# Performance work log

Measured on AMD Instinct MI355X. Metric: run time of the kernel, lower is better.

## Reference

```python
import jax, jax.numpy as jnp
import numpy as np

TS = 7           # tile_size
STRIDE = 3       # tile_size - overlap
RATIO = 4
C = 4            # margs.channel
S_LR = 256       # ms side
S_HR = 1024      # margs.test_sidelen
N_ATOMS = 10
TSR = TS * RATIO
STR_R = STRIDE * RATIO
NP_SIDE = (S_LR - TS) // STRIDE + 1   # 84 (pad_size == 0 for this config)
NPATCH = NP_SIDE ** 2                 # 7056


def unfold(x, k, stride):
    # x: [1,C,H,W] -> [1, C*k*k, N]  (channel-major patch layout, same as torch F.unfold)
    p = jax.lax.conv_general_dilated_patches(x, (k, k), (stride, stride), 'VALID')
    return p.reshape(1, p.shape[1], -1)


def fold(p, c, h, w, k, stride):
    # F.fold is the adjoint (overlap-add transpose) of unfold
    _, vjp = jax.vjp(lambda x: unfold(x, k, stride), jnp.zeros((1, c, h, w), p.dtype))
    return vjp(p)[0]


def _gauss(k, sigma):
    ax = np.arange(k) - (k - 1) / 2.0
    g = np.exp(-ax ** 2 / (2.0 * sigma ** 2))
    g = g / g.sum()
    return jnp.asarray(np.outer(g, g), dtype=jnp.float32)


def wald(x, ratio):
    # wald_protocol low-pass: depthwise gaussian blur (MTF approximation)
    k = 4 * ratio + 1
    ker = jnp.broadcast_to(_gauss(k, float(ratio)), (x.shape[1], 1, k, k))
    return jax.lax.conv_general_dilated(x, ker, (1, 1), 'SAME', feature_group_count=x.shape[1])


def setup_inputs() -> dict:
    key = jax.random.key(0)
    ks = jax.random.split(key, 4)
    # histogram-matched PAN high-pass (C channels, matched per band)
    pan_hp = jax.random.normal(ks[0], (1, C, S_HR, S_HR), jnp.float32)
    lr_pan_hp = wald(pan_hp, RATIO)[:, :, 2:-1:4, 2:-1:4]          # [1,C,256,256]
    lr_dict = unfold(lr_pan_hp, TS, STRIDE)[0].T                    # [NPATCH, C*TS^2]
    hr_dict = unfold(pan_hp, TSR, STR_R)[0].T                       # [NPATCH, C*TSR^2]
    ms_hp = 0.1 * jax.random.normal(ks[1], (1, C, S_LR, S_LR), jnp.float32)
    lms = jax.random.normal(ks[2], (1, C, S_HR, S_HR), jnp.float32)
    hrms_hp = 0.1 * jax.random.normal(ks[3], (1, C, S_HR, S_HR), jnp.float32)
    divisor = fold(jnp.ones((1, C * TSR * TSR, NPATCH), jnp.float32), C, S_HR, S_HR, TSR, STR_R)
    divisor = jnp.where(divisor == 0, 1.0, divisor)
    return {"hrms_hp": hrms_hp, "ms_hp": ms_hp, "lms": lms,
            "lr_dict": lr_dict, "hr_dict": hr_dict, "divisor": divisor}


def reference(hrms_hp, ms_hp, lms, lr_dict, hr_dict, divisor):
    N = lr_dict.shape[0]
    hw = TS * TS
    hwr = TSR * TSR
    # residual MS patches: ms_hp - degraded current estimate
    lr_hrms = wald(hrms_hp, RATIO)[:, :, 2:-1:4, 2:-1:4]
    res_ms = unfold(ms_hp - lr_hrms, TS, STRIDE)[0]                 # [C*hw, N]
    res_ms = res_ms.reshape(C, hw, N).transpose(2, 0, 1).reshape(N * C, hw)  # '(n c) hw'
    res = res_ms.reshape(N, C * hw)                                 # 'n (c hw)'
    idx_cols = [jnp.arange(N)]                                      # index[:,0] = arange
    alpha = None
    for i in range(N_ATOMS):
        if i > 0:
            # greedy atom selection: max |<residual, atom>|
            idx_cols.append(jnp.argmax(jnp.abs(res @ lr_dict.T), axis=-1))
        idx = jnp.stack(idx_cols, axis=1)                           # [N, i+1]
        A = lr_dict[idx]                                            # [N, i+1, C*hw]
        A = A.reshape(N, i + 1, C, hw).transpose(0, 2, 3, 1).reshape(N * C, hw, i + 1)
        # batched least squares (min-norm, matches torch.linalg.lstsq)
        alpha = jnp.einsum('bij,bj->bi', jnp.linalg.pinv(A), res_ms)  # [N*C, i+1]
        res = (res_ms - jnp.einsum('bi,bpi->bp', alpha, A)).reshape(N, C * hw)
    idx = jnp.stack(idx_cols, axis=1)                               # [N, N_ATOMS]
    Hd = hr_dict[idx].reshape(N, N_ATOMS, C, hwr).transpose(0, 2, 1, 3).reshape(N * C, N_ATOMS, hwr)
    hr_p = jnp.einsum('bi,bip->bp', alpha, Hd)                      # [N*C, hwr]
    hr_p = hr_p.reshape(N, C, hwr).transpose(1, 2, 0).reshape(1, C * hwr, N)
    hrms_out = fold(hr_p, C, S_HR, S_HR, TSR, STR_R) / (divisor + 1e-8) + hrms_hp
    return hrms_out + lms
```

## Files before the change

### kernel.cpp

```cpp
#include <hip/hip_runtime.h>
#include <math.h>

#define NP    7056
#define NP2   7168
#define NPS   84
#define CCH   4
#define HW    49
#define HWR   784
#define KF    196
#define KSEG  196
#define KC    608
#define NH    19
#define NA    10
#define SLR   256
#define GK    17

typedef _Float16 half8 __attribute__((ext_vector_type(8)));
typedef float f32x4 __attribute__((ext_vector_type(4)));

__global__ void hpass_kernel(const float* __restrict__ hr, float* __restrict__ htmp) {
    __shared__ float g[GK];
    int tid = threadIdx.x;
    if (tid < GK) {
        double s = 0.0, mine = 0.0;
        for (int k = 0; k < GK; k++) {
            double ax = (double)k - 8.0;
            double e = exp(-ax * ax / 32.0);
            s += e;
            if (k == tid) mine = e;
        }
        g[tid] = (float)(mine / s);
    }
    __syncthreads();
    int gid = blockIdx.x * 256 + tid;
    int xs = gid & 255;
    int y  = (gid >> 8) & 1023;
    int c  = gid >> 18;
    const float* row = hr + (size_t)(c * 1024 + y) * 1024;
    int xb = xs * 4 - 6;
    float acc = 0.f;
#pragma unroll
    for (int k = 0; k < GK; k++) {
        int xc = xb + k;
        float v = (xc >= 0 && xc < 1024) ? row[xc] : 0.f;
        acc = fmaf(g[k], v, acc);
    }
    htmp[gid] = acc;
}

__global__ void vpass_kernel(const float* __restrict__ htmp, const float* __restrict__ ms,
                             float* __restrict__ diff) {
    __shared__ float g[GK];
    int tid = threadIdx.x;
    if (tid < GK) {
        double s = 0.0, mine = 0.0;
        for (int k = 0; k < GK; k++) {
            double ax = (double)k - 8.0;
            double e = exp(-ax * ax / 32.0);
            s += e;
            if (k == tid) mine = e;
        }
        g[tid] = (float)(mine / s);
    }
    __syncthreads();
    int gid = blockIdx.x * 256 + tid;
    int xs = gid & 255;
    int ys = (gid >> 8) & 255;
    int c  = gid >> 16;
    int yb = ys * 4 - 6;
    float acc = 0.f;
#pragma unroll
    for (int k = 0; k < GK; k++) {
        int yc = yb + k;
        float v = (yc >= 0 && yc < 1024) ? htmp[(size_t)(c * 1024 + yc) * 256 + xs] : 0.f;
        acc = fmaf(g[k], v, acc);
    }
    diff[gid] = ms[gid] - acc;
}

__global__ void build_y_kernel(const float* __restrict__ diff, float* __restrict__ yb) {
    int gid = blockIdx.x * 256 + threadIdx.x;
    if (gid >= NP * CCH * HW) return;
    int p = gid % HW;
    int b = gid / HW;
    int c = b & 3;
    int n = b >> 2;
    int py = n / NPS, px = n % NPS;
    int dy = p / 7, dx = p % 7;
    yb[gid] = diff[(size_t)(c * SLR + py * 3 + dy) * SLR + px * 3 + dx];
}

__global__ void splitcat_kernel(const float* __restrict__ src, _Float16* __restrict__ Dcat) {
    int gid = blockIdx.x * 256 + threadIdx.x;
    int r = gid / 76, v8 = gid - r * 76;
    const float* srow = src + (size_t)r * KF;
    bool valid = (r < NP);
    half8 o;
#pragma unroll
    for (int e = 0; e < 8; e++) {
        int k = v8 * 8 + e;
        int seg = (k >= 392) ? 2 : (k >= 196 ? 1 : 0);
        int ks = k - seg * 196;
        float x = (valid && k < 588) ? srow[ks] : 0.f;
        _Float16 hi = (_Float16)x;
        o[e] = (seg == 1) ? (_Float16)(x - (float)hi) : hi;
    }
    *(half8*)&Dcat[(size_t)r * KC + v8 * 8] = o;
}

__global__ void hd16_kernel(const float* __restrict__ hr_dict, _Float16* __restrict__ hd) {
    int gid = blockIdx.x * 256 + threadIdx.x;
    if (gid >= (NP * CCH * HWR) / 8) return;
    const float4 a = *(const float4*)&hr_dict[(size_t)gid * 8];
    const float4 b = *(const float4*)&hr_dict[(size_t)gid * 8 + 4];
    half8 o;
    o[0] = (_Float16)a.x; o[1] = (_Float16)a.y; o[2] = (_Float16)a.z; o[3] = (_Float16)a.w;
    o[4] = (_Float16)b.x; o[5] = (_Float16)b.y; o[6] = (_Float16)b.z; o[7] = (_Float16)b.w;
    *(half8*)&hd[(size_t)gid * 8] = o;
}

__device__ __forceinline__ unsigned long long shfl_xor_u64(unsigned long long v, int m) {
    unsigned int lo = (unsigned int)v;
    unsigned int hi = (unsigned int)(v >> 32);
    lo = __shfl_xor(lo, m, 64);
    hi = __shfl_xor(hi, m, 64);
    return ((unsigned long long)hi << 32) | (unsigned long long)lo;
}

__device__ __forceinline__ void gload16(const void* g, void* l) {
    __builtin_amdgcn_global_load_lds((const __attribute__((address_space(1))) void*)(void*)g,
                                     (__attribute__((address_space(3))) void*)l, 16, 0, 0);
}

__global__ __launch_bounds__(512, 4) void mfma_argmax_kernel(
    const _Float16* __restrict__ Rcat, const _Float16* __restrict__ Dcat,
    unsigned long long* __restrict__ keys, int seg) {
    __shared__ __align__(16) _Float16 lds[3 * 12288];
    const int tid = threadIdx.x;
    const int lane = tid & 63;
    const int wave = tid >> 6;
    const int wm = wave >> 1;
    const int wn = wave & 1;

    int b0 = (int)blockIdx.x;
    int xcd = b0 & 7, w = b0 >> 3;
    int by = w % 28;
    int bx = xcd * 7 + w / 28;
    const int row0 = by * 256, col0 = bx * 128;

    const int lr = lane & 15, lk = lane >> 4;
    const int xk = (lk ^ ((lr >> 1) & 3)) * 8;
    const int aBase = (wm * 64 + lr) * 32 + xk;
    const int bBase = 8192 + (wn * 64 + lr) * 32 + xk;

    const int srow = wave * 16 + (lane >> 2);
    const int sc = ((lane & 3) ^ ((lane >> 3) & 3)) * 8;
    const _Float16* pA = Rcat + (size_t)(row0 + srow) * KC + sc;
    const _Float16* pB = Dcat + (size_t)(col0 + srow) * KC + sc;
    const int dA1 = wave * 512, dA2 = 4096 + wave * 512, dB = 8192 + wave * 512;

    auto STAGE = [&](int h) {
        int q = (h % 3) * 12288;
        int off = h * 32;
        gload16(pA + off, &lds[q + dA1]);
        gload16(pA + (size_t)128 * KC + off, &lds[q + dA2]);
        gload16(pB + off, &lds[q + dB]);
    };

    f32x4 acc[4][4];
#pragma unroll
    for (int u = 0; u < 4; u++)
#pragma unroll
        for (int v = 0; v < 4; v++) {
            f32x4 zz = {0.f, 0.f, 0.f, 0.f};
            acc[u][v] = zz;
        }

    STAGE(0);
    STAGE(1);

    for (int h = 0; h < NH; ++h) {
        const int q = (h % 3) * 12288;
        int hn = h + 2; if (hn > NH - 1) hn = NH - 1;

        asm volatile("s_waitcnt vmcnt(3)" ::: "memory");
        __builtin_amdgcn_s_barrier();

        STAGE(hn);

        half8 aF[4], bF[4];
#pragma unroll
        for (int u = 0; u < 4; ++u)
            aF[u] = *(const half8*)&lds[q + aBase + u * 512];
#pragma unroll
        for (int v = 0; v < 4; ++v)
            bF[v] = *(const half8*)&lds[q + bBase + v * 512];

        __builtin_amdgcn_s_setprio(1);
#pragma unroll
        for (int u = 0; u < 4; ++u)
#pragma unroll
            for (int v = 0; v < 4; ++v)
                acc[u][v] = __builtin_amdgcn_mfma_f32_16x16x32_f16(aF[u], bF[v], acc[u][v], 0, 0, 0);
        __builtin_amdgcn_s_setprio(0);

        asm volatile("s_waitcnt lgkmcnt(0)" ::: "memory");
    }
    asm volatile("s_waitcnt vmcnt(0)" ::: "memory");

    unsigned long long* kseg = keys + (size_t)seg * NP;
#pragma unroll
    for (int u = 0; u < 4; u++)
#pragma unroll
        for (int j = 0; j < 4; j++) {
            unsigned long long key = 0ull;
#pragma unroll
            for (int v = 0; v < 4; v++) {
                int gc = col0 + wn * 64 + v * 16 + lr;
                if (gc < NP) {
                    unsigned int bits = __float_as_uint(fabsf(acc[u][v][j]));
                    unsigned long long k2 = ((unsigned long long)bits << 32) |
                                            (unsigned long long)(0xFFFFFFFFu - (unsigned int)gc);
                    key = (k2 > key) ? k2 : key;
                }
            }
#pragma unroll
            for (int m = 1; m < 16; m <<= 1) {
                unsigned long long o = shfl_xor_u64(key, m);
                key = (o > key) ? o : key;
            }
            if (lr == 0) {
                int gr = row0 + wm * 64 + u * 16 + lk * 4 + j;
                if (gr < NP) atomicMax(kseg + gr, key);
            }
        }
}

template <int M>
__global__ __launch_bounds__(256) void solve_kernel(
    const float* __restrict__ yb, const float* __restrict__ dict,
    const unsigned long long* __restrict__ keys9,
    int* __restrict__ idxb, float* __restrict__ alphab,
    _Float16* __restrict__ Rcat) {
    int n = (blockIdx.x * 256 + threadIdx.x) >> 6;
    int lane = threadIdx.x & 63;
    int g = lane >> 4, t = lane & 15;

    int newidx = 0;
    if (M >= 2) newidx = (int)(0xFFFFFFFFu -
        (unsigned int)(keys9[(size_t)(M - 2) * NP + n] & 0xFFFFFFFFull));
    if (lane == 0) {
        if (M == 1) idxb[n * NA] = n;
        else        idxb[n * NA + (M - 1)] = newidx;
    }

    int id[M];
#pragma unroll
    for (int k = 0; k < M; k++)
        id[k] = (k == 0) ? n : ((M >= 2 && k == M - 1) ? newidx : idxb[n * NA + k]);

    const int b = n * CCH + g;
    const int base_c = g * HW;

    constexpr int TRI = M * (M + 1) / 2;
    float G[TRI];
    float rhs[M];
#pragma unroll
    for (int q = 0; q < TRI; q++) G[q] = 0.f;
#pragma unroll
    for (int k = 0; k < M; k++) rhs[k] = 0.f;

#pragma unroll
    for (int rep = 0; rep < 4; rep++) {
        int p = t + rep * 16;
        if (p < HW) {
            float a[M];
#pragma unroll
            for (int k = 0; k < M; k++)
                a[k] = dict[(size_t)id[k] * KF + base_c + p];
            float yp = yb[(size_t)b * HW + p];
#pragma unroll
            for (int k = 0; k < M; k++) {
                rhs[k] = fmaf(a[k], yp, rhs[k]);
#pragma unroll
                for (int l = 0; l <= k; l++)
                    G[k * (k + 1) / 2 + l] = fmaf(a[k], a[l], G[k * (k + 1) / 2 + l]);
            }
        }
    }

#pragma unroll
    for (int m = 1; m < 16; m <<= 1) {
#pragma unroll
        for (int q = 0; q < TRI; q++) G[q] += __shfl_xor(G[q], m, 64);
#pragma unroll
        for (int k = 0; k < M; k++) rhs[k] += __shfl_xor(rhs[k], m, 64);
    }

#pragma unroll
    for (int k = 0; k < M; k++) {
        float s = G[k * (k + 1) / 2 + k];
#pragma unroll
        for (int j = 0; j < k; j++) {
            float l = G[k * (k + 1) / 2 + j];
            s = fmaf(-l, l, s);
        }
        float inv = 1.0f / sqrtf(fmaxf(s, 1e-30f));
        G[k * (k + 1) / 2 + k] = inv;
#pragma unroll
        for (int r = k + 1; r < M; r++) {
            float tt = G[r * (r + 1) / 2 + k];
#pragma unroll
            for (int j = 0; j < k; j++)
                tt = fmaf(-G[r * (r + 1) / 2 + j], G[k * (k + 1) / 2 + j], tt);
            G[r * (r + 1) / 2 + k] = tt * inv;
        }
    }
#pragma unroll
    for (int k = 0; k < M; k++) {
        float tt = rhs[k];
#pragma unroll
        for (int j = 0; j < k; j++) tt = fmaf(-G[k * (k + 1) / 2 + j], rhs[j], tt);
        rhs[k] = tt * G[k * (k + 1) / 2 + k];
    }
#pragma unroll
    for (int k = M - 1; k >= 0; k--) {
        float tt = rhs[k];
#pragma unroll
        for (int j = k + 1; j < M; j++) tt = fmaf(-G[j * (j + 1) / 2 + k], rhs[j], tt);
        rhs[k] = tt * G[k * (k + 1) / 2 + k];
    }

    if (t == 0) {
#pragma unroll
        for (int k = 0; k < M; k++) alphab[(size_t)b * NA + k] = rhs[k];
    }

    if (M < NA) {
        _Float16* r0 = Rcat + (size_t)n * KC + base_c;
#pragma unroll
        for (int rep = 0; rep < 4; rep++) {
            int p = t + rep * 16;
            if (p < HW) {
                float s = yb[(size_t)b * HW + p];
#pragma unroll
                for (int k = 0; k < M; k++)
                    s = fmaf(-rhs[k], dict[(size_t)id[k] * KF + base_c + p], s);
                _Float16 hi = (_Float16)s;
                r0[p] = hi;
                r0[KSEG + p] = hi;
                r0[2 * KSEG + p] = (_Float16)(s - (float)hi);
            }
        }
    }
}

__global__ __launch_bounds__(256) void recon_kernel(
    const float* __restrict__ alphab, const int* __restrict__ idxb,
    const _Float16* __restrict__ hd, _Float16* __restrict__ hr_p) {
    int n = blockIdx.x;
    int tid = threadIdx.x;
    __shared__ float al[CCH * NA];
    __shared__ int idn[NA];
    if (tid < CCH * NA) al[tid] = alphab[(size_t)n * CCH * NA + tid];
    if (tid < NA) idn[tid] = idxb[n * NA + tid];
    __syncthreads();
    for (int v = tid; v < (CCH * HWR) / 8; v += 256) {
        int c = v / (HWR / 8);
        float s[8] = {0.f, 0.f, 0.f, 0.f, 0.f, 0.f, 0.f, 0.f};
#pragma unroll
        for (int k = 0; k < NA; k++) {
            half8 d = *(const half8*)&hd[(size_t)idn[k] * (CCH * HWR) + v * 8];
            float ak = al[c * NA + k];
#pragma unroll
            for (int e = 0; e < 8; e++) s[e] = fmaf(ak, (float)d[e], s[e]);
        }
        half8 o;
#pragma unroll
        for (int e = 0; e < 8; e++) o[e] = (_Float16)s[e];
        *(half8*)&hr_p[(size_t)n * (CCH * HWR) + v * 8] = o;
    }
}

__global__ __launch_bounds__(256) void fold2_kernel(
    const _Float16* __restrict__ hr_p, const float* __restrict__ divisor,
    const float* __restrict__ hrms, const float* __restrict__ lms,
    float* __restrict__ out) {
    int gid = blockIdx.x * 256 + threadIdx.x;
    int x  = gid & 1023;
    int yy = (gid >> 10) & 1023;
    int c  = gid >> 20;

    int t0 = yy - 27;
    int py0 = (t0 > 0) ? (t0 + 11) / 12 : 0;
    int py1 = min(83, yy / 12);
    int s0 = x - 27;
    int px0 = (s0 > 0) ? (s0 + 11) / 12 : 0;
    int px1 = min(83, x / 12);

    float acc = 0.f;
    for (int py = py0; py <= py1; py++) {
        int qy = yy - py * 12;
        for (int px = px0; px <= px1; px++) {
            int qx = x - px * 12;
            int n = py * NPS + px;
            acc += (float)hr_p[(size_t)n * (CCH * HWR) + c * HWR + qy * 28 + qx];
        }
    }
    out[gid] = acc / (divisor[gid] + 1e-8f) + hrms[gid] + lms[gid];
}

__global__ __launch_bounds__(256) void fold_final_kernel(
    const float* __restrict__ alphab, const int* __restrict__ idxb,
    const float* __restrict__ hr_dict, const float* __restrict__ divisor,
    const float* __restrict__ hrms, const float* __restrict__ lms,
    float* __restrict__ out) {
    int gid = blockIdx.x * 256 + threadIdx.x;
    int x  = gid & 1023;
    int yy = (gid >> 10) & 1023;
    int c  = gid >> 20;
    int t0 = yy - 27;
    int py0 = (t0 > 0) ? (t0 + 11) / 12 : 0;
    int py1 = min(83, yy / 12);
    int s0 = x - 27;
    int px0 = (s0 > 0) ? (s0 + 11) / 12 : 0;
    int px1 = min(83, x / 12);
    float acc = 0.f;
    for (int py = py0; py <= py1; py++) {
        int qy = yy - py * 12;
        for (int px = px0; px <= px1; px++) {
            int qx = x - px * 12;
            int n = py * NPS + px;
            const float* al = alphab + (size_t)(n * CCH + c) * NA;
            const int* idn = idxb + n * NA;
            int q = qy * 28 + qx;
            float s = 0.f;
#pragma unroll
            for (int k = 0; k < NA; k++)
                s = fmaf(al[k], hr_dict[(size_t)idn[k] * (CCH * HWR) + c * HWR + q], s);
            acc += s;
        }
    }
    out[gid] = acc / (divisor[gid] + 1e-8f) + hrms[gid] + lms[gid];
}

extern "C" void kernel_launch(void* const* d_in, const int* in_sizes, int n_in,
                              void* d_out, int out_size, void* d_ws, size_t ws_size,
                              hipStream_t stream) {
    const float* hrms    = (const float*)d_in[0];
    const float* ms      = (const float*)d_in[1];
    const float* lms     = (const float*)d_in[2];
    const float* lr_dict = (const float*)d_in[3];
    const float* hr_dict = (const float*)d_in[4];
    const float* divisor = (const float*)d_in[5];
    float* out = (float*)d_out;

    char* ws = (char*)d_ws;
    size_t off = 0;
    auto alloc = [&](size_t bytes) -> void* {
        void* p = ws + off;
        off += (bytes + 255) & ~(size_t)255;
        return p;
    };
    float* htmp   = (float*)alloc((size_t)4 * 1024 * 256 * 4);
    float* diff   = (float*)alloc((size_t)4 * 256 * 256 * 4);
    float* yb     = (float*)alloc((size_t)NP * CCH * HW * 4);
    float* alphab = (float*)alloc((size_t)NP * CCH * NA * 4);
    int*   idxb   = (int*)alloc((size_t)NP * NA * 4);
    unsigned long long* keys9 = (unsigned long long*)alloc((size_t)NP * 9 * 8);
    _Float16* Dcat = (_Float16*)alloc((size_t)NP2 * KC * 2);
    _Float16* Rcat = (_Float16*)alloc((size_t)NP2 * KC * 2);
    _Float16* hd16 = (_Float16*)alloc((size_t)NP * CCH * HWR * 2);
    _Float16* hr_p = (_Float16*)alloc((size_t)NP * CCH * HWR * 2);
    bool two_stage = (off <= ws_size);

    hpass_kernel<<<4096, 256, 0, stream>>>(hrms, htmp);
    vpass_kernel<<<1024, 256, 0, stream>>>(htmp, ms, diff);
    build_y_kernel<<<(NP * CCH * HW + 255) / 256, 256, 0, stream>>>(diff, yb);
    splitcat_kernel<<<(NP2 * 76) / 256, 256, 0, stream>>>(lr_dict, Dcat);
    hipMemsetAsync(keys9, 0, (size_t)NP * 9 * 8, stream);
    if (two_stage)
        hd16_kernel<<<((NP * CCH * HWR) / 8 + 255) / 256, 256, 0, stream>>>(hr_dict, hd16);

    int sblocks = NP / 4;
    for (int i = 0; i < NA; i++) {
        if (i > 0)
            mfma_argmax_kernel<<<1568, 512, 0, stream>>>(Rcat, Dcat, keys9, i - 1);
        switch (i + 1) {
            case 1:  solve_kernel<1><<<sblocks, 256, 0, stream>>>(yb, lr_dict, keys9, idxb, alphab, Rcat); break;
            case 2:  solve_kernel<2><<<sblocks, 256, 0, stream>>>(yb, lr_dict, keys9, idxb, alphab, Rcat); break;
            case 3:  solve_kernel<3><<<sblocks, 256, 0, stream>>>(yb, lr_dict, keys9, idxb, alphab, Rcat); break;
            case 4:  solve_kernel<4><<<sblocks, 256, 0, stream>>>(yb, lr_dict, keys9, idxb, alphab, Rcat); break;
            case 5:  solve_kernel<5><<<sblocks, 256, 0, stream>>>(yb, lr_dict, keys9, idxb, alphab, Rcat); break;
            case 6:  solve_kernel<6><<<sblocks, 256, 0, stream>>>(yb, lr_dict, keys9, idxb, alphab, Rcat); break;
            case 7:  solve_kernel<7><<<sblocks, 256, 0, stream>>>(yb, lr_dict, keys9, idxb, alphab, Rcat); break;
            case 8:  solve_kernel<8><<<sblocks, 256, 0, stream>>>(yb, lr_dict, keys9, idxb, alphab, Rcat); break;
            case 9:  solve_kernel<9><<<sblocks, 256, 0, stream>>>(yb, lr_dict, keys9, idxb, alphab, Rcat); break;
            case 10: solve_kernel<10><<<sblocks, 256, 0, stream>>>(yb, lr_dict, keys9, idxb, alphab, Rcat); break;
        }
    }

    if (two_stage) {
        recon_kernel<<<NP, 256, 0, stream>>>(alphab, idxb, hd16, hr_p);
        fold2_kernel<<<(4 * 1024 * 1024) / 256, 256, 0, stream>>>(hr_p, divisor, hrms, lms, out);
    } else {
        fold_final_kernel<<<(4 * 1024 * 1024) / 256, 256, 0, stream>>>(
            alphab, idxb, hr_dict, divisor, hrms, lms, out);
    }
}
```

Baseline: 1.089 ms.

## Load A fragments directly from global into registers, stage only B in LDS

The argmax GEMM kernel stops staging the residual (A) tile through LDS. Each wave now loads its A fragments straight from global memory into registers one k-step ahead, while only the dictionary (B) tile goes through a triple-buffered LDS ring via global_load_lds. LDS use per block drops from 3x12288 to 3x4096 halves, which cuts LDS traffic and may allow more resident blocks. The cost is uncoalesced global reads for A, with each row read by both wn waves, and the wait counts and sched barriers have to keep the prefetch ordering correct.

```diff
diff --git a/kernel.cpp b/kernel.cpp
--- a/kernel.cpp
+++ b/kernel.cpp
@@ -135,7 +135,7 @@
 __global__ __launch_bounds__(512, 4) void mfma_argmax_kernel(
     const _Float16* __restrict__ Rcat, const _Float16* __restrict__ Dcat,
     unsigned long long* __restrict__ keys, int seg) {
-    __shared__ __align__(16) _Float16 lds[3 * 12288];
+    __shared__ __align__(16) _Float16 lds[3 * 4096];
     const int tid = threadIdx.x;
     const int lane = tid & 63;
     const int wave = tid >> 6;
@@ -150,21 +150,23 @@
 
     const int lr = lane & 15, lk = lane >> 4;
     const int xk = (lk ^ ((lr >> 1) & 3)) * 8;
-    const int aBase = (wm * 64 + lr) * 32 + xk;
-    const int bBase = 8192 + (wn * 64 + lr) * 32 + xk;
-
-    const int srow = wave * 16 + (lane >> 2);
-    const int sc = ((lane & 3) ^ ((lane >> 3) & 3)) * 8;
-    const _Float16* pA = Rcat + (size_t)(row0 + srow) * KC + sc;
-    const _Float16* pB = Dcat + (size_t)(col0 + srow) * KC + sc;
-    const int dA1 = wave * 512, dA2 = 4096 + wave * 512, dB = 8192 + wave * 512;
-
-    auto STAGE = [&](int h) {
-        int q = (h % 3) * 12288;
-        int off = h * 32;
-        gload16(pA + off, &lds[q + dA1]);
-        gload16(pA + (size_t)128 * KC + off, &lds[q + dA2]);
-        gload16(pB + off, &lds[q + dB]);
+    const int bBase = (wn * 64 + lr) * 32 + xk;
+
+    const _Float16* pAfrag = Rcat + (size_t)(row0 + wm * 64 + lr) * KC + lk * 8;
+
+    const int sc = ((tid & 3) ^ ((tid >> 3) & 3)) * 8;
+    const _Float16* pB = Dcat + (size_t)(col0 + (tid >> 2)) * KC + sc;
+    const int dB = tid * 8;
+
+    auto STAGE_B = [&](int h) {
+        gload16(pB + h * 32, &lds[(h % 3) * 4096 + dB]);
+    };
+
+    half8 aF[4];
+    auto LOADA = [&](int h) {
+#pragma unroll
+        for (int u = 0; u < 4; ++u)
+            aF[u] = *(const half8*)(pAfrag + (size_t)u * 16 * KC + h * 32);
     };
 
     f32x4 acc[4][4];
@@ -176,22 +178,17 @@
             acc[u][v] = zz;
         }
 
-    STAGE(0);
-    STAGE(1);
+    STAGE_B(0);
+    LOADA(0);
+    STAGE_B(1);
 
     for (int h = 0; h < NH; ++h) {
-        const int q = (h % 3) * 12288;
-        int hn = h + 2; if (hn > NH - 1) hn = NH - 1;
-
-        asm volatile("s_waitcnt vmcnt(3)" ::: "memory");
+        const int q = (h % 3) * 4096;
+
+        asm volatile("s_waitcnt vmcnt(5)" ::: "memory");
         __builtin_amdgcn_s_barrier();
 
-        STAGE(hn);
-
-        half8 aF[4], bF[4];
-#pragma unroll
-        for (int u = 0; u < 4; ++u)
-            aF[u] = *(const half8*)&lds[q + aBase + u * 512];
+        half8 bF[4];
 #pragma unroll
         for (int v = 0; v < 4; ++v)
             bF[v] = *(const half8*)&lds[q + bBase + v * 512];
@@ -203,6 +200,13 @@
             for (int v = 0; v < 4; ++v)
                 acc[u][v] = __builtin_amdgcn_mfma_f32_16x16x32_f16(aF[u], bF[v], acc[u][v], 0, 0, 0);
         __builtin_amdgcn_s_setprio(0);
+        __builtin_amdgcn_sched_barrier(0);
+
+        int hn1 = h + 1; if (hn1 > NH - 1) hn1 = NH - 1;
+        LOADA(hn1);
+        __builtin_amdgcn_sched_barrier(0);
+        int hn2 = h + 2; if (hn2 > NH - 1) hn2 = NH - 1;
+        STAGE_B(hn2);
 
         asm volatile("s_waitcnt lgkmcnt(0)" ::: "memory");
     }
```

Result: slower. 1.277 ms (+17.2%).
